# Performance work log

Hardware: AMD Instinct MI355X
Metric: run time of the kernel (lower is better)

Reference implementation:

```python
import jax, jax.numpy as jnp
import numpy as np

HIDDEN = 1024
HEADS = 16
HEAD_DIM = HIDDEN // HEADS


def setup_inputs() -> dict:
    key = jax.random.key(0)
    ks = jax.random.split(key, 8)
    B, S = 2, 2048
    scale = 1.0 / np.sqrt(HIDDEN)
    return {
        "hidden_states": jax.random.normal(ks[0], (B, S, HIDDEN), dtype=jnp.float32),
        "attention_mask": jax.random.randint(ks[1], (B, S), 0, 2, dtype=jnp.int32),
        "Wq": jax.random.normal(ks[2], (HIDDEN, HIDDEN), dtype=jnp.float32) * scale,
        "bq": jax.random.normal(ks[3], (HIDDEN,), dtype=jnp.float32) * 0.02,
        "Wk": jax.random.normal(ks[4], (HIDDEN, HIDDEN), dtype=jnp.float32) * scale,
        "bk": jax.random.normal(ks[5], (HIDDEN,), dtype=jnp.float32) * 0.02,
        "Wv": jax.random.normal(ks[6], (HIDDEN, HIDDEN), dtype=jnp.float32) * scale,
        "bv": jax.random.normal(ks[7], (HIDDEN,), dtype=jnp.float32) * 0.02,
    }


def _split_heads(x):
    # [B, S, H*D] -> [B, H, S, D]
    B, S, _ = x.shape
    return x.reshape(B, S, HEADS, HEAD_DIM).transpose(0, 2, 1, 3)


def reference(hidden_states, attention_mask, Wq, bq, Wk, bk, Wv, bv):
    B, S, _ = hidden_states.shape
    q = _split_heads(hidden_states @ Wq + bq) / jnp.sqrt(jnp.asarray(HEAD_DIM, hidden_states.dtype))
    k = _split_heads(hidden_states @ Wk + bk)
    v = _split_heads(hidden_states @ Wv + bv)
    # scores: [B, H, S, S]
    scores = jnp.einsum("bhqd,bhkd->bhqk", q, k).astype(jnp.float32)
    mask = attention_mask[:, None, None, :]  # [B,1,1,S]
    scores = jnp.where(mask == 0, jnp.float32(-1e8), scores)
    probs = jax.nn.softmax(scores, axis=-1).astype(v.dtype)
    ctx = jnp.einsum("bhqk,bhkd->bhqd", probs, v)
    return ctx.transpose(0, 2, 1, 3).reshape(B, S, HIDDEN)
```

## Files before the change

### kernel.cpp

```cpp
#include <hip/hip_runtime.h>
#include <math.h>

typedef __attribute__((ext_vector_type(4))) float f32x4;
typedef __attribute__((ext_vector_type(16))) float f32x16;
typedef _Float16 f16x8 __attribute__((ext_vector_type(8)));
typedef __fp16 fp16x2 __attribute__((ext_vector_type(2)));
typedef unsigned int uintv2 __attribute__((ext_vector_type(2)));

#define MFMA16(a, b, c) __builtin_amdgcn_mfma_f32_16x16x32_f16((a), (b), (c), 0, 0, 0)
#define MFMA32(a, b, c) __builtin_amdgcn_mfma_f32_32x32x16_f16((a), (b), (c), 0, 0, 0)

__device__ __forceinline__ unsigned short f2h(float f) {
    union { _Float16 h; unsigned short u; } v; v.h = (_Float16)f; return v.u;
}
__device__ __forceinline__ unsigned pk2f(float a, float b) {
    union { fp16x2 h; unsigned u; } v; v.h = __builtin_amdgcn_cvt_pkrtz(a, b); return v.u;
}

#if defined(__has_builtin)
#if __has_builtin(__builtin_amdgcn_global_load_lds)
#define HAVE_GLL 1
#endif
#endif

__device__ __forceinline__ void gload16(const void* g, void* lds) {
#ifdef HAVE_GLL
    __builtin_amdgcn_global_load_lds(
        (const __attribute__((address_space(1))) void*)g,
        (__attribute__((address_space(3))) void*)lds, 16, 0, 0);
#else
    *(f16x8*)lds = *(const f16x8*)g;
#endif
}

__global__ __launch_bounds__(256) void prep_kernel(
    const float* __restrict__ X, const float* __restrict__ Wq,
    const float* __restrict__ Wk, const float* __restrict__ Wv,
    const int* __restrict__ mask,
    unsigned short* __restrict__ XF, unsigned short* __restrict__ WT,
    int* __restrict__ kpos, int* __restrict__ kept,
    float* __restrict__ cmask_c) {
    __shared__ float T[64][65];
    __shared__ int wsum[4];
    __shared__ int ktot;
    const int bid = blockIdx.x, t = threadIdx.x;
    if (bid < 4096) {
        int i = (bid * 256 + t) * 4;
        float4 v = *reinterpret_cast<const float4*>(X + i);
        ushort4 h;
        h.x = f2h(v.x); h.y = f2h(v.y); h.z = f2h(v.z); h.w = f2h(v.w);
        *reinterpret_cast<ushort4*>(XF + i) = h;
        return;
    }
    if (bid >= 4864) {
        const int b = bid - 4864;
        const int lane = t & 63, wv = t >> 6;
        const int i0 = b * 2048 + t * 8;
        int mv[8];
        {
            int4 ma = *reinterpret_cast<const int4*>(mask + i0);
            int4 mb = *reinterpret_cast<const int4*>(mask + i0 + 4);
            mv[0] = ma.x != 0; mv[1] = ma.y != 0; mv[2] = ma.z != 0; mv[3] = ma.w != 0;
            mv[4] = mb.x != 0; mv[5] = mb.y != 0; mv[6] = mb.z != 0; mv[7] = mb.w != 0;
        }
        int s = 0;
#pragma unroll
        for (int j = 0; j < 8; ++j) s += mv[j];
        int v = s;
#pragma unroll
        for (int off = 1; off < 64; off <<= 1) {
            int o = __shfl_up(v, off);
            if (lane >= off) v += o;
        }
        if (lane == 63) wsum[wv] = v;
        __syncthreads();
        int woff = 0;
        for (int i = 0; i < wv; ++i) woff += wsum[i];
        const int incl = v + woff;
        int p = incl - s;
#pragma unroll
        for (int j = 0; j < 8; ++j) { kpos[i0 + j] = p; p += mv[j]; }
        if (t == 255) { ktot = incl; kept[b] = incl; }
        __syncthreads();
        const int kt = ktot;
#pragma unroll
        for (int j = 0; j < 8; ++j)
            cmask_c[i0 + j] = (t * 8 + j < kt) ? -13.f : -1e9f;
        return;
    }
    const int t2 = bid - 4096;
    const int z = t2 >> 8, rem = t2 & 255;
    const int k0 = (rem & 15) * 64, n0 = (rem >> 4) * 64;
    const float* W = (z == 0) ? Wq : ((z == 1) ? Wk : Wv);
    unsigned short* Wo = WT + (size_t)z * 1024 * 1024;
    for (int i = 0; i < 4; i++) {
        int fid = t + i * 256;
        int rr = fid >> 4, cc = fid & 15;
        float4 v = *reinterpret_cast<const float4*>(W + (size_t)(k0 + rr) * 1024 + n0 + cc * 4);
        T[rr][cc * 4 + 0] = v.x; T[rr][cc * 4 + 1] = v.y;
        T[rr][cc * 4 + 2] = v.z; T[rr][cc * 4 + 3] = v.w;
    }
    __syncthreads();
    for (int i = 0; i < 4; i++) {
        int e = t + i * 256;
        int n = e >> 4, kq = (e & 15) * 4;
        ushort4 h;
        h.x = f2h(T[kq + 0][n]); h.y = f2h(T[kq + 1][n]);
        h.z = f2h(T[kq + 2][n]); h.w = f2h(T[kq + 3][n]);
        size_t o = (size_t)(n0 + n) * 1024 + k0 + kq;
        *reinterpret_cast<ushort4*>(Wo + o) = h;
    }
}

__global__ __launch_bounds__(256, 3) void qkv_gemm_kernel(
    const unsigned short* __restrict__ XF, const unsigned short* __restrict__ WT,
    const float* __restrict__ bq, const float* __restrict__ bk,
    const float* __restrict__ bv, const int* __restrict__ mask,
    const int* __restrict__ kpos,
    unsigned short* __restrict__ QF, unsigned short* __restrict__ KF,
    unsigned short* __restrict__ VT) {
    __shared__ __align__(16) char smem[3][2][8192];
    int z = blockIdx.z;
    const unsigned short* Wz = WT + (size_t)z * 1024 * 1024;
    const float* bias = (z == 0) ? bq : ((z == 1) ? bk : bv);
    const int m0 = blockIdx.x * 128, n0 = blockIdx.y * 128;
    const int tid = threadIdx.x, lane = tid & 63, wid = tid >> 6;
    const int wr = wid >> 1, wc = wid & 1;
    const int g = lane >> 4, r16 = lane & 15;

    f32x4 acc[4][4] = {};

#define QSTAGE(BUFI, K0)                                                             \
    {                                                                                \
        _Pragma("unroll")                                                            \
        for (int p = 0; p < 2; ++p) {                                                \
            int row = p * 64 + (tid >> 2);                                           \
            int ec = ((tid & 3) ^ (row & 3)) * 8;                                    \
            size_t xo = (size_t)(m0 + row) * 1024 + (K0) + ec;                       \
            size_t wo = (size_t)(n0 + row) * 1024 + (K0) + ec;                       \
            gload16(XF + xo, &smem[(BUFI)][0][0] + p * 4096 + tid * 16);             \
            gload16(Wz + wo, &smem[(BUFI)][1][0] + p * 4096 + tid * 16);             \
        }                                                                            \
    }

    QSTAGE(0, 0);
    QSTAGE(1, 32);
    int bufc = 0, bufs = 2;
    for (int ki = 0; ki < 32; ++ki) {
        if (ki < 31) {
            asm volatile("s_waitcnt vmcnt(4)" ::: "memory");
        } else {
            asm volatile("s_waitcnt vmcnt(0)" ::: "memory");
        }
        __builtin_amdgcn_s_barrier();
        if (ki < 30) QSTAGE(bufs, (ki + 2) * 32);
        const char* bX = &smem[bufc][0][0];
        const char* bW = &smem[bufc][1][0];
        const int sx = (r16 & 3) << 4;

        f16x8 af[4], bf[4];
#pragma unroll
        for (int mi = 0; mi < 4; ++mi)
            af[mi] = *(const f16x8*)(bX + (wr * 64 + mi * 16 + r16) * 64 + ((g << 4) ^ sx));
#pragma unroll
        for (int ni = 0; ni < 4; ++ni)
            bf[ni] = *(const f16x8*)(bW + (wc * 64 + ni * 16 + r16) * 64 + ((g << 4) ^ sx));
        __builtin_amdgcn_s_setprio(1);
#pragma unroll
        for (int mi = 0; mi < 4; ++mi)
#pragma unroll
            for (int ni = 0; ni < 4; ++ni)
                acc[mi][ni] = MFMA16(af[mi], bf[ni], acc[mi][ni]);
        __builtin_amdgcn_s_setprio(0);
        bufc = (bufc == 2) ? 0 : bufc + 1;
        bufs = (bufs == 2) ? 0 : bufs + 1;
    }

#pragma unroll
    for (int mi = 0; mi < 4; ++mi)
#pragma unroll
        for (int r = 0; r < 4; ++r) {
            int m = m0 + wr * 64 + mi * 16 + g * 4 + r;
            int b = m >> 11, s = m & 2047;
            int keep = 1, spos = s;
            if (z != 0) {
                keep = mask[b * 2048 + s];
                spos = kpos[b * 2048 + s];
            }
            if (z != 0 && !keep) continue;
#pragma unroll
            for (int ni = 0; ni < 4; ++ni) {
                int n = n0 + wc * 64 + ni * 16 + r16;
                float val = acc[mi][ni][r] + bias[n];
                if (z == 0) val *= 0.18033688011112042f;
                int hh = n >> 6, d = n & 63;
                unsigned short hv = f2h(val);
                if (z == 0)
                    QF[((size_t)(b * 16 + hh) * 2048 + s) * 64 + d] = hv;
                else if (z == 1)
                    KF[((size_t)(b * 16 + hh) * 2048 + spos) * 64 + d] = hv;
                else
                    VT[((size_t)(b * 16 + hh) * 64 + d) * 2048 + spos] = hv;
            }
        }
}

__global__ __launch_bounds__(256, 4) void attn_kernel(
    const unsigned short* __restrict__ QF, const unsigned short* __restrict__ KF,
    const unsigned short* __restrict__ VT, const float* __restrict__ cmask_c,
    const int* __restrict__ kept, float* __restrict__ out) {
    __shared__ __align__(16) char smem[2][2][8192];
    __shared__ __align__(16) float cmlds[2048];
    const int tid = threadIdx.x;
    const int lane = tid & 63, wid = tid >> 6;
    const int hi = lane >> 5, l31 = lane & 31;
    const int bid = blockIdx.x;
    const int wgid = (bid & 7) * 128 + (bid >> 3);
    const int bh = wgid >> 5, qb = wgid & 31;
    const int b = bh >> 4, h = bh & 15;
    const int qh = wid & 1, kh = wid >> 1;
    const size_t base = (size_t)bh * 2048 * 64;
    const unsigned short* KFh = KF + base;
    const unsigned short* VTh = VT + base;
    const int qrow = qb * 64 + qh * 32 + l31;
    const int swz = (l31 & 7) << 4;
    const int kt = kept[b];
    const int nch = (kt + 63) >> 6;

    f16x8 qf[4];
#pragma unroll
    for (int ks = 0; ks < 4; ++ks)
        qf[ks] = *reinterpret_cast<const f16x8*>(QF + base + (size_t)qrow * 64 + ks * 16 + hi * 8);

    const int lr = lane >> 3, c16 = lane & 7;
    const int gce = (c16 ^ lr) << 3;
    const int pl = wid >> 1, half = wid & 1;
    const unsigned short* mys = pl ? VTh : KFh;
    const int rstr = pl ? 2048 : 64;

    f32x16 ctx[2] = {};
    float l_st = 0.f;

#define STAGE(BUFI, K0)                                                              \
    {                                                                                \
        char* dst = &smem[(BUFI)][pl][0] + half * 4096;                              \
        size_t koff = pl ? (size_t)(K0) : (size_t)(K0) * 64;                         \
        _Pragma("unroll")                                                            \
        for (int i = 0; i < 4; ++i) {                                                \
            int r = half * 32 + i * 8 + lr;                                          \
            gload16(mys + koff + (size_t)r * rstr + gce, dst + i * 1024 + lane * 16);\
        }                                                                            \
    }

    STAGE(0, 0);
    {
        float4 c0 = *reinterpret_cast<const float4*>(cmask_c + b * 2048 + tid * 8);
        float4 c1 = *reinterpret_cast<const float4*>(cmask_c + b * 2048 + tid * 8 + 4);
        *reinterpret_cast<float4*>(&cmlds[tid * 8]) = c0;
        *reinterpret_cast<float4*>(&cmlds[tid * 8 + 4]) = c1;
    }

    for (int ch = 0; ch < nch; ++ch) {
        asm volatile("s_waitcnt vmcnt(0) lgkmcnt(0)" ::: "memory");
        __builtin_amdgcn_s_barrier();
        if (ch + 1 < nch) STAGE((ch + 1) & 1, (ch + 1) * 64);
        const int buf = ch & 1;
        const char* bK = &smem[buf][0][0];
        const char* bV = &smem[buf][1][0];
        const int k0s = ch * 64 + kh * 32;

        f32x16 sc;
        {
            const char* rK = bK + (kh * 32 + l31) * 128;
            f32x16 a = {};
            __builtin_amdgcn_s_setprio(1);
#pragma unroll
            for (int ks = 0; ks < 4; ++ks)
                a = MFMA32(*(const f16x8*)(rK + ((ks * 32 + hi * 16) ^ swz)), qf[ks], a);
            __builtin_amdgcn_s_setprio(0);
            sc = a;
        }

        float p[16];
        float psum = 0.f;
#pragma unroll
        for (int G = 0; G < 4; ++G) {
            float4 cv = *reinterpret_cast<const float4*>(&cmlds[k0s + 8 * G + 4 * hi]);
            int bo = G * 4;
            float e0 = __builtin_amdgcn_exp2f(sc[bo + 0] + cv.x);
            float e1 = __builtin_amdgcn_exp2f(sc[bo + 1] + cv.y);
            float e2 = __builtin_amdgcn_exp2f(sc[bo + 2] + cv.z);
            float e3 = __builtin_amdgcn_exp2f(sc[bo + 3] + cv.w);
            p[bo + 0] = e0; p[bo + 1] = e1; p[bo + 2] = e2; p[bo + 3] = e3;
            psum += e0 + e1 + e2 + e3;
        }
        l_st += psum;

        f16x8 pf[2];
        {
            unsigned a0 = pk2f(p[0], p[1]),   a1 = pk2f(p[2], p[3]);
            unsigned b0 = pk2f(p[4], p[5]),   b1 = pk2f(p[6], p[7]);
            unsigned c0 = pk2f(p[8], p[9]),   c1 = pk2f(p[10], p[11]);
            unsigned d0 = pk2f(p[12], p[13]), d1 = pk2f(p[14], p[15]);
            uintv2 r0 = __builtin_amdgcn_permlane32_swap(a0, b0, false, false);
            uintv2 r1 = __builtin_amdgcn_permlane32_swap(a1, b1, false, false);
            uintv2 r2 = __builtin_amdgcn_permlane32_swap(c0, d0, false, false);
            uintv2 r3 = __builtin_amdgcn_permlane32_swap(c1, d1, false, false);
            union { unsigned u[4]; f16x8 v; } f0, f1;
            f0.u[0] = r0[0]; f0.u[1] = r1[0]; f0.u[2] = r0[1]; f0.u[3] = r1[1];
            f1.u[0] = r2[0]; f1.u[1] = r3[0]; f1.u[2] = r2[1]; f1.u[3] = r3[1];
            pf[0] = f0.v; pf[1] = f1.v;
        }

        __builtin_amdgcn_s_setprio(1);
#pragma unroll
        for (int dt = 0; dt < 2; ++dt) {
            const char* rV = bV + (dt * 32 + l31) * 128;
            f32x16 a = ctx[dt];
#pragma unroll
            for (int ks = 0; ks < 2; ++ks)
                a = MFMA32(*(const f16x8*)(rV + ((kh * 64 + ks * 32 + hi * 16) ^ swz)), pf[ks], a);
            ctx[dt] = a;
        }
        __builtin_amdgcn_s_setprio(0);
    }

    l_st += __shfl_xor(l_st, 32);
    asm volatile("s_waitcnt lgkmcnt(0)" ::: "memory");
    __builtin_amdgcn_s_barrier();
    float* scr = (float*)&smem[0][0][0];
    if (kh) {
        float* dst = scr + qh * 2304 + lane * 36;
#pragma unroll
        for (int dt = 0; dt < 2; ++dt)
#pragma unroll
            for (int G = 0; G < 4; ++G) {
                float4 st;
                st.x = ctx[dt][G * 4 + 0]; st.y = ctx[dt][G * 4 + 1];
                st.z = ctx[dt][G * 4 + 2]; st.w = ctx[dt][G * 4 + 3];
                *reinterpret_cast<float4*>(dst + dt * 16 + G * 4) = st;
            }
        scr[4608 + qh * 64 + lane] = l_st;
        asm volatile("s_waitcnt lgkmcnt(0)" ::: "memory");
    }
    __builtin_amdgcn_s_barrier();
    if (!kh) {
        const float* src = scr + qh * 2304 + lane * 36;
        float l_full = l_st + scr[4608 + qh * 64 + lane];
        float inv_l = 1.0f / l_full;
        size_t ob0 = ((size_t)b * 2048 + qrow) * 1024 + h * 64 + 4 * hi;
#pragma unroll
        for (int dt = 0; dt < 2; ++dt)
#pragma unroll
            for (int G = 0; G < 4; ++G) {
                float4 pv = *reinterpret_cast<const float4*>(src + dt * 16 + G * 4);
                float4 st;
                st.x = (ctx[dt][G * 4 + 0] + pv.x) * inv_l;
                st.y = (ctx[dt][G * 4 + 1] + pv.y) * inv_l;
                st.z = (ctx[dt][G * 4 + 2] + pv.z) * inv_l;
                st.w = (ctx[dt][G * 4 + 3] + pv.w) * inv_l;
                *reinterpret_cast<float4*>(out + ob0 + dt * 32 + 8 * G) = st;
            }
    }
}

extern "C" void kernel_launch(void* const* d_in, const int* in_sizes, int n_in,
                              void* d_out, int out_size, void* d_ws, size_t ws_size,
                              hipStream_t stream) {
    const float* X  = (const float*)d_in[0];
    const int* mask = (const int*)d_in[1];
    const float* Wq = (const float*)d_in[2];
    const float* bq = (const float*)d_in[3];
    const float* Wk = (const float*)d_in[4];
    const float* bk = (const float*)d_in[5];
    const float* Wv = (const float*)d_in[6];
    const float* bv = (const float*)d_in[7];
    float* out = (float*)d_out;

    char* ws = (char*)d_ws;
    const size_t SZ_X = (size_t)4096 * 1024 * 2;
    const size_t SZ_W = (size_t)1024 * 1024 * 2;
    const size_t SZ_Q = (size_t)2 * 16 * 2048 * 64 * 2;
    unsigned short* XF = (unsigned short*)(ws);
    unsigned short* WT = (unsigned short*)(ws + SZ_X);
    unsigned short* QF = (unsigned short*)(ws + SZ_X + 3 * SZ_W);
    unsigned short* KF = (unsigned short*)(ws + SZ_X + 3 * SZ_W + 1 * SZ_Q);
    unsigned short* VT = (unsigned short*)(ws + SZ_X + 3 * SZ_W + 2 * SZ_Q);
    char* extra = ws + SZ_X + 3 * SZ_W + 3 * SZ_Q;
    int* KPOS   = (int*)(extra);
    int* KEPT   = (int*)(extra + 16384);
    float* CMC  = (float*)(extra + 16384 + 256);

    prep_kernel<<<4866, 256, 0, stream>>>(X, Wq, Wk, Wv, mask, XF, WT, KPOS, KEPT, CMC);
    qkv_gemm_kernel<<<dim3(32, 8, 3), 256, 0, stream>>>(XF, WT, bq, bk, bv, mask, KPOS,
                                                        QF, KF, VT);
    attn_kernel<<<1024, 256, 0, stream>>>(QF, KF, VT, CMC, KEPT, out);
}
```

Baseline: 96.16 us.

## Move masked key compaction out of QKV GEMM epilogue into separate gather kernel

```diff
diff --git a/kernel.cpp b/kernel.cpp
--- a/kernel.cpp
+++ b/kernel.cpp
@@ -38,7 +38,7 @@
     const float* __restrict__ Wk, const float* __restrict__ Wv,
     const int* __restrict__ mask,
     unsigned short* __restrict__ XF, unsigned short* __restrict__ WT,
-    int* __restrict__ kpos, int* __restrict__ kept,
+    int* __restrict__ sel, int* __restrict__ kept,
     float* __restrict__ cmask_c) {
     __shared__ float T[64][65];
     __shared__ int wsum[4];
@@ -79,7 +79,10 @@
         const int incl = v + woff;
         int p = incl - s;
 #pragma unroll
-        for (int j = 0; j < 8; ++j) { kpos[i0 + j] = p; p += mv[j]; }
+        for (int j = 0; j < 8; ++j) {
+            if (mv[j]) sel[b * 2048 + p] = t * 8 + j;
+            p += mv[j];
+        }
         if (t == 255) { ktot = incl; kept[b] = incl; }
         __syncthreads();
         const int kt = ktot;
@@ -115,8 +118,7 @@
 __global__ __launch_bounds__(256, 3) void qkv_gemm_kernel(
     const unsigned short* __restrict__ XF, const unsigned short* __restrict__ WT,
     const float* __restrict__ bq, const float* __restrict__ bk,
-    const float* __restrict__ bv, const int* __restrict__ mask,
-    const int* __restrict__ kpos,
+    const float* __restrict__ bv,
     unsigned short* __restrict__ QF, unsigned short* __restrict__ KF,
     unsigned short* __restrict__ VT) {
     __shared__ __align__(16) char smem[3][2][8192];
@@ -179,35 +181,63 @@
 #pragma unroll
     for (int mi = 0; mi < 4; ++mi)
 #pragma unroll
-        for (int r = 0; r < 4; ++r) {
-            int m = m0 + wr * 64 + mi * 16 + g * 4 + r;
-            int b = m >> 11, s = m & 2047;
-            int keep = 1, spos = s;
-            if (z != 0) {
-                keep = mask[b * 2048 + s];
-                spos = kpos[b * 2048 + s];
-            }
-            if (z != 0 && !keep) continue;
-#pragma unroll
-            for (int ni = 0; ni < 4; ++ni) {
+        for (int ni = 0; ni < 4; ++ni)
+#pragma unroll
+            for (int r = 0; r < 4; ++r) {
+                int m = m0 + wr * 64 + mi * 16 + g * 4 + r;
                 int n = n0 + wc * 64 + ni * 16 + r16;
                 float val = acc[mi][ni][r] + bias[n];
                 if (z == 0) val *= 0.18033688011112042f;
-                int hh = n >> 6, d = n & 63;
+                int b = m >> 11, s = m & 2047, hh = n >> 6, d = n & 63;
                 unsigned short hv = f2h(val);
-                if (z == 0)
-                    QF[((size_t)(b * 16 + hh) * 2048 + s) * 64 + d] = hv;
-                else if (z == 1)
-                    KF[((size_t)(b * 16 + hh) * 2048 + spos) * 64 + d] = hv;
-                else
-                    VT[((size_t)(b * 16 + hh) * 64 + d) * 2048 + spos] = hv;
+                if (z == 2) {
+                    VT[((size_t)(b * 16 + hh) * 64 + d) * 2048 + s] = hv;
+                } else {
+                    size_t o = ((size_t)(b * 16 + hh) * 2048 + s) * 64 + d;
+                    if (z == 0) QF[o] = hv; else KF[o] = hv;
+                }
             }
-        }
+}
+
+__global__ __launch_bounds__(256) void compact_kernel(
+    const unsigned short* __restrict__ KF, const unsigned short* __restrict__ VT,
+    const int* __restrict__ sel, const int* __restrict__ kept,
+    unsigned short* __restrict__ KC, unsigned short* __restrict__ VC) {
+    const int bid = blockIdx.x, t = threadIdx.x;
+    if (bid < 2048) {
+        const int bh = bid >> 6, rg = bid & 63;
+        const int b = bh >> 4;
+        const int j = rg * 32 + (t >> 3), l8 = t & 7;
+        if (j >= kept[b]) return;
+        const int s = sel[b * 2048 + j];
+        *(f16x8*)(KC + ((size_t)bh * 2048 + j) * 64 + l8 * 8) =
+            *(const f16x8*)(KF + ((size_t)bh * 2048 + s) * 64 + l8 * 8);
+        return;
+    }
+    const int v = bid - 2048;
+    const int bh = v >> 6, d = v & 63;
+    const int b = bh >> 4;
+    const int kt = kept[b];
+    const int kpad = (kt + 63) & ~63;
+    const int j0 = t * 8;
+    if (j0 >= kpad) return;
+    const unsigned short* src = VT + ((size_t)bh * 64 + d) * 2048;
+    int4 s0 = *reinterpret_cast<const int4*>(sel + b * 2048 + j0);
+    int4 s1 = *reinterpret_cast<const int4*>(sel + b * 2048 + j0 + 4);
+    int si[8] = {s0.x, s0.y, s0.z, s0.w, s1.x, s1.y, s1.z, s1.w};
+    union { unsigned short o[8]; f16x8 v8; } ov;
+#pragma unroll
+    for (int i = 0; i < 8; ++i) {
+        int j = j0 + i;
+        int s = (j < kt) ? si[i] : 0;
+        ov.o[i] = (j < kt) ? src[s] : (unsigned short)0;
+    }
+    *(f16x8*)(VC + ((size_t)bh * 64 + d) * 2048 + j0) = ov.v8;
 }
 
 __global__ __launch_bounds__(256, 4) void attn_kernel(
-    const unsigned short* __restrict__ QF, const unsigned short* __restrict__ KF,
-    const unsigned short* __restrict__ VT, const float* __restrict__ cmask_c,
+    const unsigned short* __restrict__ QF, const unsigned short* __restrict__ KC,
+    const unsigned short* __restrict__ VC, const float* __restrict__ cmask_c,
     const int* __restrict__ kept, float* __restrict__ out) {
     __shared__ __align__(16) char smem[2][2][8192];
     __shared__ __align__(16) float cmlds[2048];
@@ -220,8 +250,8 @@
     const int b = bh >> 4, h = bh & 15;
     const int qh = wid & 1, kh = wid >> 1;
     const size_t base = (size_t)bh * 2048 * 64;
-    const unsigned short* KFh = KF + base;
-    const unsigned short* VTh = VT + base;
+    const unsigned short* KFh = KC + base;
+    const unsigned short* VTh = VC + base;
     const int qrow = qb * 64 + qh * 32 + l31;
     const int swz = (l31 & 7) << 4;
     const int kt = kept[b];
@@ -386,13 +416,15 @@
     unsigned short* QF = (unsigned short*)(ws + SZ_X + 3 * SZ_W);
     unsigned short* KF = (unsigned short*)(ws + SZ_X + 3 * SZ_W + 1 * SZ_Q);
     unsigned short* VT = (unsigned short*)(ws + SZ_X + 3 * SZ_W + 2 * SZ_Q);
-    char* extra = ws + SZ_X + 3 * SZ_W + 3 * SZ_Q;
-    int* KPOS   = (int*)(extra);
+    unsigned short* KC = (unsigned short*)(ws + SZ_X + 3 * SZ_W + 3 * SZ_Q);
+    unsigned short* VC = (unsigned short*)(ws + SZ_X + 3 * SZ_W + 4 * SZ_Q);
+    char* extra = ws + SZ_X + 3 * SZ_W + 5 * SZ_Q;
+    int* SEL    = (int*)(extra);
     int* KEPT   = (int*)(extra + 16384);
     float* CMC  = (float*)(extra + 16384 + 256);
 
-    prep_kernel<<<4866, 256, 0, stream>>>(X, Wq, Wk, Wv, mask, XF, WT, KPOS, KEPT, CMC);
-    qkv_gemm_kernel<<<dim3(32, 8, 3), 256, 0, stream>>>(XF, WT, bq, bk, bv, mask, KPOS,
-                                                        QF, KF, VT);
-    attn_kernel<<<1024, 256, 0, stream>>>(QF, KF, VT, CMC, KEPT, out);
-}
+    prep_kernel<<<4866, 256, 0, stream>>>(X, Wq, Wk, Wv, mask, XF, WT, SEL, KEPT, CMC);
+    qkv_gemm_kernel<<<dim3(32, 8, 3), 256, 0, stream>>>(XF, WT, bq, bk, bv, QF, KF, VT);
+    compact_kernel<<<4096, 256, 0, stream>>>(KF, VT, SEL, KEPT, KC, VC);
+    attn_kernel<<<1024, 256, 0, stream>>>(QF, KC, VC, CMC, KEPT, out);
+}
```

After: 93.76 us. 1.03x faster.

## Compact kept rows of X before K/V projection to skip masked-row GEMM work

Applied to the files above, without the earlier changes.

```diff
diff --git a/kernel.cpp b/kernel.cpp
--- a/kernel.cpp
+++ b/kernel.cpp
@@ -38,7 +38,7 @@
     const float* __restrict__ Wk, const float* __restrict__ Wv,
     const int* __restrict__ mask,
     unsigned short* __restrict__ XF, unsigned short* __restrict__ WT,
-    int* __restrict__ kpos, int* __restrict__ kept,
+    int* __restrict__ sel, int* __restrict__ kept,
     float* __restrict__ cmask_c) {
     __shared__ float T[64][65];
     __shared__ int wsum[4];
@@ -79,7 +79,10 @@
         const int incl = v + woff;
         int p = incl - s;
 #pragma unroll
-        for (int j = 0; j < 8; ++j) { kpos[i0 + j] = p; p += mv[j]; }
+        for (int j = 0; j < 8; ++j) {
+            if (mv[j]) sel[b * 2048 + p] = t * 8 + j;
+            p += mv[j];
+        }
         if (t == 255) { ktot = incl; kept[b] = incl; }
         __syncthreads();
         const int kt = ktot;
@@ -112,18 +115,43 @@
     }
 }
 
+__global__ __launch_bounds__(256) void gather_xc_kernel(
+    const unsigned short* __restrict__ XF, const int* __restrict__ sel,
+    const int* __restrict__ kept, unsigned short* __restrict__ XC) {
+    const int x = blockIdx.x, t = threadIdx.x;
+    const int b = x >> 11, j = x & 2047;
+    if (j >= kept[b]) return;
+    const int s = sel[b * 2048 + j];
+    const unsigned short* src = XF + ((size_t)b * 2048 + s) * 1024;
+    unsigned short* dst = XC + ((size_t)b * 2048 + j) * 1024;
+    *reinterpret_cast<ushort4*>(dst + t * 4) =
+        *reinterpret_cast<const ushort4*>(src + t * 4);
+}
+
 __global__ __launch_bounds__(256, 3) void qkv_gemm_kernel(
-    const unsigned short* __restrict__ XF, const unsigned short* __restrict__ WT,
+    const unsigned short* __restrict__ XF, const unsigned short* __restrict__ XC,
+    const unsigned short* __restrict__ WT,
     const float* __restrict__ bq, const float* __restrict__ bk,
-    const float* __restrict__ bv, const int* __restrict__ mask,
-    const int* __restrict__ kpos,
-    unsigned short* __restrict__ QF, unsigned short* __restrict__ KF,
-    unsigned short* __restrict__ VT) {
+    const float* __restrict__ bv, const int* __restrict__ kept,
+    unsigned short* __restrict__ QF, unsigned short* __restrict__ KC,
+    unsigned short* __restrict__ VC) {
     __shared__ __align__(16) char smem[3][2][8192];
-    int z = blockIdx.z;
+    const int z = blockIdx.z;
     const unsigned short* Wz = WT + (size_t)z * 1024 * 1024;
     const float* bias = (z == 0) ? bq : ((z == 1) ? bk : bv);
-    const int m0 = blockIdx.x * 128, n0 = blockIdx.y * 128;
+    const int n0 = blockIdx.y * 128;
+    int bb = 0, mb0;
+    const unsigned short* Xs;
+    if (z == 0) {
+        mb0 = blockIdx.x * 128;
+        Xs = XF;
+    } else {
+        bb = blockIdx.x >> 4;
+        mb0 = (blockIdx.x & 15) * 128;
+        const int kneed = (kept[bb] + 63) & ~63;
+        if (mb0 >= kneed) return;
+        Xs = XC + (size_t)bb * 2048 * 1024;
+    }
     const int tid = threadIdx.x, lane = tid & 63, wid = tid >> 6;
     const int wr = wid >> 1, wc = wid & 1;
     const int g = lane >> 4, r16 = lane & 15;
@@ -136,9 +164,9 @@
         for (int p = 0; p < 2; ++p) {                                                \
             int row = p * 64 + (tid >> 2);                                           \
             int ec = ((tid & 3) ^ (row & 3)) * 8;                                    \
-            size_t xo = (size_t)(m0 + row) * 1024 + (K0) + ec;                       \
+            size_t xo = (size_t)(mb0 + row) * 1024 + (K0) + ec;                      \
             size_t wo = (size_t)(n0 + row) * 1024 + (K0) + ec;                       \
-            gload16(XF + xo, &smem[(BUFI)][0][0] + p * 4096 + tid * 16);             \
+            gload16(Xs + xo, &smem[(BUFI)][0][0] + p * 4096 + tid * 16);             \
             gload16(Wz + wo, &smem[(BUFI)][1][0] + p * 4096 + tid * 16);             \
         }                                                                            \
     }
@@ -179,35 +207,29 @@
 #pragma unroll
     for (int mi = 0; mi < 4; ++mi)
 #pragma unroll
-        for (int r = 0; r < 4; ++r) {
-            int m = m0 + wr * 64 + mi * 16 + g * 4 + r;
-            int b = m >> 11, s = m & 2047;
-            int keep = 1, spos = s;
-            if (z != 0) {
-                keep = mask[b * 2048 + s];
-                spos = kpos[b * 2048 + s];
-            }
-            if (z != 0 && !keep) continue;
-#pragma unroll
-            for (int ni = 0; ni < 4; ++ni) {
+        for (int ni = 0; ni < 4; ++ni)
+#pragma unroll
+            for (int r = 0; r < 4; ++r) {
+                int m = mb0 + wr * 64 + mi * 16 + g * 4 + r;
                 int n = n0 + wc * 64 + ni * 16 + r16;
                 float val = acc[mi][ni][r] + bias[n];
                 if (z == 0) val *= 0.18033688011112042f;
                 int hh = n >> 6, d = n & 63;
                 unsigned short hv = f2h(val);
-                if (z == 0)
+                if (z == 0) {
+                    int b = m >> 11, s = m & 2047;
                     QF[((size_t)(b * 16 + hh) * 2048 + s) * 64 + d] = hv;
-                else if (z == 1)
-                    KF[((size_t)(b * 16 + hh) * 2048 + spos) * 64 + d] = hv;
-                else
-                    VT[((size_t)(b * 16 + hh) * 64 + d) * 2048 + spos] = hv;
+                } else if (z == 1) {
+                    KC[((size_t)(bb * 16 + hh) * 2048 + m) * 64 + d] = hv;
+                } else {
+                    VC[((size_t)(bb * 16 + hh) * 64 + d) * 2048 + m] = hv;
+                }
             }
-        }
 }
 
 __global__ __launch_bounds__(256, 4) void attn_kernel(
-    const unsigned short* __restrict__ QF, const unsigned short* __restrict__ KF,
-    const unsigned short* __restrict__ VT, const float* __restrict__ cmask_c,
+    const unsigned short* __restrict__ QF, const unsigned short* __restrict__ KC,
+    const unsigned short* __restrict__ VC, const float* __restrict__ cmask_c,
     const int* __restrict__ kept, float* __restrict__ out) {
     __shared__ __align__(16) char smem[2][2][8192];
     __shared__ __align__(16) float cmlds[2048];
@@ -220,8 +242,8 @@
     const int b = bh >> 4, h = bh & 15;
     const int qh = wid & 1, kh = wid >> 1;
     const size_t base = (size_t)bh * 2048 * 64;
-    const unsigned short* KFh = KF + base;
-    const unsigned short* VTh = VT + base;
+    const unsigned short* KFh = KC + base;
+    const unsigned short* VTh = VC + base;
     const int qrow = qb * 64 + qh * 32 + l31;
     const int swz = (l31 & 7) << 4;
     const int kt = kept[b];
@@ -384,15 +406,17 @@
     unsigned short* XF = (unsigned short*)(ws);
     unsigned short* WT = (unsigned short*)(ws + SZ_X);
     unsigned short* QF = (unsigned short*)(ws + SZ_X + 3 * SZ_W);
-    unsigned short* KF = (unsigned short*)(ws + SZ_X + 3 * SZ_W + 1 * SZ_Q);
-    unsigned short* VT = (unsigned short*)(ws + SZ_X + 3 * SZ_W + 2 * SZ_Q);
-    char* extra = ws + SZ_X + 3 * SZ_W + 3 * SZ_Q;
-    int* KPOS   = (int*)(extra);
+    unsigned short* KC = (unsigned short*)(ws + SZ_X + 3 * SZ_W + 1 * SZ_Q);
+    unsigned short* VC = (unsigned short*)(ws + SZ_X + 3 * SZ_W + 2 * SZ_Q);
+    unsigned short* XC = (unsigned short*)(ws + SZ_X + 3 * SZ_W + 3 * SZ_Q);
+    char* extra = ws + SZ_X + 3 * SZ_W + 4 * SZ_Q;
+    int* SEL    = (int*)(extra);
     int* KEPT   = (int*)(extra + 16384);
     float* CMC  = (float*)(extra + 16384 + 256);
 
-    prep_kernel<<<4866, 256, 0, stream>>>(X, Wq, Wk, Wv, mask, XF, WT, KPOS, KEPT, CMC);
-    qkv_gemm_kernel<<<dim3(32, 8, 3), 256, 0, stream>>>(XF, WT, bq, bk, bv, mask, KPOS,
-                                                        QF, KF, VT);
-    attn_kernel<<<1024, 256, 0, stream>>>(QF, KF, VT, CMC, KEPT, out);
-}
+    prep_kernel<<<4866, 256, 0, stream>>>(X, Wq, Wk, Wv, mask, XF, WT, SEL, KEPT, CMC);
+    gather_xc_kernel<<<4096, 256, 0, stream>>>(XF, SEL, KEPT, XC);
+    qkv_gemm_kernel<<<dim3(32, 8, 3), 256, 0, stream>>>(XF, XC, WT, bq, bk, bv, KEPT,
+                                                        QF, KC, VC);
+    attn_kernel<<<1024, 256, 0, stream>>>(QF, KC, VC, CMC, KEPT, out);
+}
```

New measurement: 89.93 us. 6.5% less time.
